# Optimization experiments

Measured on AMD Instinct MI355X. Metric: run time of the kernel, lower is better.

Reference implementation:

```python
import jax, jax.numpy as jnp
import numpy as np

B, C, H, Wd = 4, 64, 64, 64


def setup_inputs() -> dict:
    key = jax.random.key(0)
    k1, k2, k3 = jax.random.split(key, 3)
    x = jax.random.normal(k1, (B, C, H, Wd), dtype=jnp.float32)
    W = jax.random.normal(k2, (C, C), dtype=jnp.float32) * (1.0 / np.sqrt(C))
    b = jax.random.normal(k3, (C,), dtype=jnp.float32) * 0.01
    return {"x": x, "W": W, "b": b}


def reference(x, W, b):
    Bz, Cz, Hz, Wz = x.shape
    N = Hz * Wz
    xf = x.reshape(Bz, Cz, N)                      # values [B,C,N]
    # shared 1x1 conv for queries and keys (same module instance in torch)
    qk = jnp.einsum('oc,bcn->bon', W, xf) + b[None, :, None]  # [B,C,N]
    # scores[b,n,m] = sum_c q[b,c,n] * k[b,c,m], scaled by 1/N
    scores = jnp.einsum('bcn,bcm->bnm', qk, qk) / N           # [B,N,N]
    attn = jax.nn.softmax(scores, axis=-1)                    # softmax over m
    # out[b,c,n] = sum_m values[b,c,m] * attn[b,n,m]
    out = jnp.einsum('bcm,bnm->bcn', xf, attn)
    return out.reshape(Bz, Cz, Hz, Wz)
```

## Files before the change

kernel.cpp:

```cpp
#include <hip/hip_runtime.h>
#include <hip/hip_bf16.h>

#define BATCH 4
#define NSP   4096

typedef __bf16 bf16x8v __attribute__((ext_vector_type(8)));
typedef __bf16 bf16x4v __attribute__((ext_vector_type(4)));
typedef float  floatx4 __attribute__((ext_vector_type(4)));

__global__ __launch_bounds__(256) void qk_kernel(const float* __restrict__ x,
                                                 const float* __restrict__ Wm,
                                                 const float* __restrict__ bias,
                                                 __bf16* __restrict__ qkT) {
    __shared__ __align__(16) __bf16 xT[64 * 72];

    const int t  = threadIdx.x;
    const int b  = blockIdx.x >> 6;
    const int n0 = (blockIdx.x & 63) << 6;

#pragma unroll
    for (int p = 0; p < 4; ++p) {
        const int c  = p * 16 + (t >> 4);
        const int n4 = (t & 15) * 4;
        const float4 v = *(const float4*)(x + (size_t)(b * 64 + c) * 4096 + n0 + n4);
        xT[(n4 + 0) * 72 + c] = (__bf16)(v.x * 0.015625f);
        xT[(n4 + 1) * 72 + c] = (__bf16)(v.y * 0.015625f);
        xT[(n4 + 2) * 72 + c] = (__bf16)(v.z * 0.015625f);
        xT[(n4 + 3) * 72 + c] = (__bf16)(v.w * 0.015625f);
    }
    __syncthreads();

    const int w = t >> 6, lane = t & 63, quad = lane >> 4, l16 = lane & 15;
    const bf16x8v a0 = *(const bf16x8v*)(xT + (w * 16 + l16) * 72 + quad * 8);
    const bf16x8v a1 = *(const bf16x8v*)(xT + (w * 16 + l16) * 72 + 32 + quad * 8);

    floatx4 acc[4];
#pragma unroll
    for (int ot = 0; ot < 4; ++ot) {
        const float* wr = Wm + (ot * 16 + l16) * 64;
        float4 wa = *(const float4*)(wr + quad * 8);
        float4 wb = *(const float4*)(wr + quad * 8 + 4);
        float4 wc = *(const float4*)(wr + 32 + quad * 8);
        float4 wd = *(const float4*)(wr + 32 + quad * 8 + 4);
        bf16x8v b0, b1;
        b0[0]=(__bf16)wa.x; b0[1]=(__bf16)wa.y; b0[2]=(__bf16)wa.z; b0[3]=(__bf16)wa.w;
        b0[4]=(__bf16)wb.x; b0[5]=(__bf16)wb.y; b0[6]=(__bf16)wb.z; b0[7]=(__bf16)wb.w;
        b1[0]=(__bf16)wc.x; b1[1]=(__bf16)wc.y; b1[2]=(__bf16)wc.z; b1[3]=(__bf16)wc.w;
        b1[4]=(__bf16)wd.x; b1[5]=(__bf16)wd.y; b1[6]=(__bf16)wd.z; b1[7]=(__bf16)wd.w;
        acc[ot] = floatx4{0.f, 0.f, 0.f, 0.f};
        acc[ot] = __builtin_amdgcn_mfma_f32_16x16x32_bf16(a0, b0, acc[ot], 0, 0, 0);
        acc[ot] = __builtin_amdgcn_mfma_f32_16x16x32_bf16(a1, b1, acc[ot], 0, 0, 0);
    }
    __syncthreads();

#pragma unroll
    for (int ot = 0; ot < 4; ++ot) {
        const float bo = bias[ot * 16 + l16] * 0.015625f;
#pragma unroll
        for (int r = 0; r < 4; ++r)
            xT[(w * 16 + quad * 4 + r) * 72 + ot * 16 + l16] = (__bf16)(acc[ot][r] + bo);
    }
    __syncthreads();

    const int n = t >> 2, seg = t & 3;
    __bf16* dst = qkT + (size_t)(b * 4096 + n0 + n) * 64 + seg * 16;
    *(bf16x8v*)dst       = *(const bf16x8v*)(xT + n * 72 + seg * 16);
    *(bf16x8v*)(dst + 8) = *(const bf16x8v*)(xT + n * 72 + seg * 16 + 8);
}

template<int SPLIT, int ITERS>
__global__ __launch_bounds__(256, 4) void attn_kernel(const float* __restrict__ x,
                                                      const __bf16* __restrict__ qkT,
                                                      __bf16* __restrict__ Opart,
                                                      float* __restrict__ Lpart) {
    __shared__ __align__(16) char smem[36864];
    __bf16* Klds = (__bf16*)smem;
    __bf16* Vlds = (__bf16*)(smem + 9216);
    __bf16* Plds = (__bf16*)(smem + 18432);
    float*  Olds = (float*)smem;

    const int t   = threadIdx.x;
    const int blk = blockIdx.x;
    const int xcd = blk & 7;
    const int b   = xcd >> 1;
    const int sub = ((blk >> 3) << 1) | (xcd & 1);
    const int qt  = sub / SPLIT;
    const int s   = sub % SPLIT;
    const int n0  = qt << 7;
    const int pblk = (b * 32 + qt) * SPLIT + s;

    const int w = t >> 6, lane = t & 63, quad = lane >> 4, l16 = lane & 15;

    bf16x8v fq[2][2];
#pragma unroll
    for (int qt2 = 0; qt2 < 2; ++qt2) {
        const __bf16* qrow = qkT + (size_t)(b * 4096 + n0 + w * 32 + qt2 * 16 + l16) * 64;
        fq[qt2][0] = *(const bf16x8v*)(qrow + quad * 8);
        fq[qt2][1] = *(const bf16x8v*)(qrow + 32 + quad * 8);
    }

    floatx4 oacc[2][4];
#pragma unroll
    for (int i = 0; i < 2; ++i)
#pragma unroll
        for (int j = 0; j < 4; ++j) oacc[i][j] = floatx4{0.f, 0.f, 0.f, 0.f};
    float rs[2] = {0.f, 0.f};

    for (int it = 0; it < ITERS; ++it) {
        const int m0 = s * (64 * ITERS) + (it << 6);
        __syncthreads();
#pragma unroll
        for (int i = 0; i < 2; ++i) {
            int idx = t + 256 * i;
            int row = idx >> 3, c8 = idx & 7;
            *(uint4*)(Klds + row * 72 + c8 * 8) =
                *(const uint4*)(qkT + (size_t)(b * 4096 + m0 + row) * 64 + c8 * 8);
        }
#pragma unroll
        for (int i = 0; i < 4; ++i) {
            int idx = t + 256 * i;
            int c = idx >> 4, f4 = idx & 15;
            const float4 v = *(const float4*)(x + (size_t)(b * 64 + c) * 4096 + m0 + f4 * 4);
            bf16x4v bv;
            bv[0] = (__bf16)v.x; bv[1] = (__bf16)v.y; bv[2] = (__bf16)v.z; bv[3] = (__bf16)v.w;
            *(bf16x4v*)(Vlds + c * 72 + f4 * 4) = bv;
        }
        __syncthreads();

#pragma unroll
        for (int mt = 0; mt < 4; ++mt) {
            const __bf16* kr = Klds + (mt * 16 + l16) * 72;
            bf16x8v ak0 = *(const bf16x8v*)(kr + quad * 8);
            bf16x8v ak1 = *(const bf16x8v*)(kr + 32 + quad * 8);
#pragma unroll
            for (int qt2 = 0; qt2 < 2; ++qt2) {
                floatx4 sT = {0.f, 0.f, 0.f, 0.f};
                sT = __builtin_amdgcn_mfma_f32_16x16x32_bf16(ak0, fq[qt2][0], sT, 0, 0, 0);
                sT = __builtin_amdgcn_mfma_f32_16x16x32_bf16(ak1, fq[qt2][1], sT, 0, 0, 0);
                float p0 = __expf(sT[0]), p1 = __expf(sT[1]);
                float p2 = __expf(sT[2]), p3 = __expf(sT[3]);
                rs[qt2] += (p0 + p1) + (p2 + p3);
                bf16x4v pv;
                pv[0] = (__bf16)p0; pv[1] = (__bf16)p1; pv[2] = (__bf16)p2; pv[3] = (__bf16)p3;
                *(bf16x4v*)(Plds + (w * 32 + qt2 * 16 + l16) * 72 + mt * 16 + quad * 4) = pv;
            }
        }

        bf16x8v ap[2][2];
#pragma unroll
        for (int qt2 = 0; qt2 < 2; ++qt2) {
            const __bf16* pr = Plds + (w * 32 + qt2 * 16 + l16) * 72;
            ap[qt2][0] = *(const bf16x8v*)(pr + quad * 8);
            ap[qt2][1] = *(const bf16x8v*)(pr + 32 + quad * 8);
        }
#pragma unroll
        for (int ct = 0; ct < 4; ++ct) {
            const __bf16* vr = Vlds + (ct * 16 + l16) * 72;
            bf16x8v bv0 = *(const bf16x8v*)(vr + quad * 8);
            bf16x8v bv1 = *(const bf16x8v*)(vr + 32 + quad * 8);
#pragma unroll
            for (int qt2 = 0; qt2 < 2; ++qt2) {
                oacc[qt2][ct] = __builtin_amdgcn_mfma_f32_16x16x32_bf16(ap[qt2][0], bv0, oacc[qt2][ct], 0, 0, 0);
                oacc[qt2][ct] = __builtin_amdgcn_mfma_f32_16x16x32_bf16(ap[qt2][1], bv1, oacc[qt2][ct], 0, 0, 0);
            }
        }
    }

#pragma unroll
    for (int qt2 = 0; qt2 < 2; ++qt2) {
        float v = rs[qt2];
        v += __shfl_xor(v, 16, 64);
        v += __shfl_xor(v, 32, 64);
        if (quad == 0)
            Lpart[(size_t)pblk * 128 + w * 32 + qt2 * 16 + l16] = v;
    }

    __syncthreads();

#pragma unroll
    for (int qt2 = 0; qt2 < 2; ++qt2)
#pragma unroll
        for (int ct = 0; ct < 4; ++ct)
#pragma unroll
            for (int r = 0; r < 4; ++r)
                Olds[(ct * 16 + l16) * 132 + w * 32 + qt2 * 16 + quad * 4 + r] = oacc[qt2][ct][r];
    __syncthreads();

    const int c = t >> 2, seg = t & 3;
#pragma unroll
    for (int i = 0; i < 4; ++i) {
        floatx4 v0 = *(const floatx4*)(Olds + c * 132 + seg * 32 + i * 8);
        floatx4 v1 = *(const floatx4*)(Olds + c * 132 + seg * 32 + i * 8 + 4);
        bf16x8v pk;
        pk[0]=(__bf16)v0[0]; pk[1]=(__bf16)v0[1]; pk[2]=(__bf16)v0[2]; pk[3]=(__bf16)v0[3];
        pk[4]=(__bf16)v1[0]; pk[5]=(__bf16)v1[1]; pk[6]=(__bf16)v1[2]; pk[7]=(__bf16)v1[3];
        *(bf16x8v*)(Opart + (size_t)pblk * 8192 + c * 128 + seg * 32 + i * 8) = pk;
    }
}

template<int SPLIT>
__global__ __launch_bounds__(256) void reduce_kernel(const __bf16* __restrict__ Opart,
                                                     const float* __restrict__ Lpart,
                                                     float* __restrict__ out) {
    const int blk = blockIdx.x;
    const int bq = blk >> 2, cq = blk & 3;
    const int b = bq >> 5, qt = bq & 31;
    const int t = threadIdx.x;
    const int c  = cq * 16 + (t >> 4);
    const int q8 = (t & 15) * 8;

    float l[8] = {0.f,0.f,0.f,0.f,0.f,0.f,0.f,0.f};
#pragma unroll
    for (int s = 0; s < SPLIT; ++s) {
        const float* lp = Lpart + ((size_t)bq * SPLIT + s) * 128 + q8;
        float4 u = *(const float4*)lp;
        float4 v = *(const float4*)(lp + 4);
        l[0]+=u.x; l[1]+=u.y; l[2]+=u.z; l[3]+=u.w;
        l[4]+=v.x; l[5]+=v.y; l[6]+=v.z; l[7]+=v.w;
    }
    float a[8] = {0.f,0.f,0.f,0.f,0.f,0.f,0.f,0.f};
#pragma unroll
    for (int s = 0; s < SPLIT; ++s) {
        bf16x8v v = *(const bf16x8v*)(Opart + ((size_t)bq * SPLIT + s) * 8192 + c * 128 + q8);
#pragma unroll
        for (int k = 0; k < 8; ++k) a[k] += (float)v[k];
    }
    float* op = out + (size_t)(b * 64 + c) * 4096 + qt * 128 + q8;
    float4 o0, o1;
    o0.x = a[0]/l[0]; o0.y = a[1]/l[1]; o0.z = a[2]/l[2]; o0.w = a[3]/l[3];
    o1.x = a[4]/l[4]; o1.y = a[5]/l[5]; o1.z = a[6]/l[6]; o1.w = a[7]/l[7];
    *(float4*)op       = o0;
    *(float4*)(op + 4) = o1;
}

extern "C" void kernel_launch(void* const* d_in, const int* in_sizes, int n_in,
                              void* d_out, int out_size, void* d_ws, size_t ws_size,
                              hipStream_t stream) {
    const float* x    = (const float*)d_in[0];
    const float* Wm   = (const float*)d_in[1];
    const float* bias = (const float*)d_in[2];
    float* out = (float*)d_out;

    char* ws = (char*)d_ws;
    __bf16* qkT = (__bf16*)ws;

    qk_kernel<<<BATCH * (NSP / 64), 256, 0, stream>>>(x, Wm, bias, qkT);

    const size_t QKT = 2097152;
    const size_t needBig = QKT + (size_t)1024 * 8192 * 2 + (size_t)1024 * 128 * 4;
    if (ws_size >= needBig) {
        __bf16* Opart = (__bf16*)(ws + QKT);
        float*  Lpart = (float*)(ws + QKT + (size_t)1024 * 8192 * 2);
        attn_kernel<8, 8><<<BATCH * 32 * 8, 256, 0, stream>>>(x, qkT, Opart, Lpart);
        reduce_kernel<8><<<512, 256, 0, stream>>>(Opart, Lpart, out);
    } else {
        __bf16* Opart = (__bf16*)(ws + QKT);
        float*  Lpart = (float*)(ws + QKT + (size_t)512 * 8192 * 2);
        attn_kernel<4, 16><<<BATCH * 32 * 4, 256, 0, stream>>>(x, qkT, Opart, Lpart);
        reduce_kernel<4><<<512, 256, 0, stream>>>(Opart, Lpart, out);
    }
}
```

Baseline: 101.4 us.

## Double-buffer K/V tiles, keep P in registers, precompute bf16 values, use exp2

The qk kernel now also writes a bf16 copy of x, so the attention kernel loads V as bf16 directly instead of converting fp32 each tile. K/V staging is double-buffered with register prefetch of the next tile, which removes one barrier per iteration. P no longer goes through LDS: the exp2 results feed the 16x16x16 MFMA directly from registers, and the log2(e) factor is folded into the q/k scale. This costs an extra workspace buffer and a second global write in qk_kernel, and it uses the older 16x16x16 MFMA shape.

```diff
diff --git a/kernel.cpp b/kernel.cpp
--- a/kernel.cpp
+++ b/kernel.cpp
@@ -4,14 +4,40 @@
 #define BATCH 4
 #define NSP   4096
 
+#define QKSCALE 0.0187675376f
+
 typedef __bf16 bf16x8v __attribute__((ext_vector_type(8)));
 typedef __bf16 bf16x4v __attribute__((ext_vector_type(4)));
+typedef short  shortx4 __attribute__((ext_vector_type(4)));
 typedef float  floatx4 __attribute__((ext_vector_type(4)));
+
+static __device__ __forceinline__ shortx4 bf4_bits(bf16x4v v) {
+    union { bf16x4v b; shortx4 s; } u; u.b = v; return u.s;
+}
+
+static __device__ __forceinline__ float fast_exp2(float x) {
+#if __has_builtin(__builtin_amdgcn_exp2f)
+    return __builtin_amdgcn_exp2f(x);
+#else
+    return exp2f(x);
+#endif
+}
+
+static __device__ __forceinline__ floatx4 mfma_pv(shortx4 a, shortx4 b, floatx4 c) {
+#if __has_builtin(__builtin_amdgcn_mfma_f32_16x16x16bf16_1k)
+    return __builtin_amdgcn_mfma_f32_16x16x16bf16_1k(a, b, c, 0, 0, 0);
+#else
+    floatx4 d;
+    asm("v_mfma_f32_16x16x16_bf16 %0, %1, %2, %3" : "=&v"(d) : "v"(a), "v"(b), "v"(c));
+    return d;
+#endif
+}
 
 __global__ __launch_bounds__(256) void qk_kernel(const float* __restrict__ x,
                                                  const float* __restrict__ Wm,
                                                  const float* __restrict__ bias,
-                                                 __bf16* __restrict__ qkT) {
+                                                 __bf16* __restrict__ qkT,
+                                                 __bf16* __restrict__ xbf) {
     __shared__ __align__(16) __bf16 xT[64 * 72];
 
     const int t  = threadIdx.x;
@@ -23,10 +49,13 @@
         const int c  = p * 16 + (t >> 4);
         const int n4 = (t & 15) * 4;
         const float4 v = *(const float4*)(x + (size_t)(b * 64 + c) * 4096 + n0 + n4);
-        xT[(n4 + 0) * 72 + c] = (__bf16)(v.x * 0.015625f);
-        xT[(n4 + 1) * 72 + c] = (__bf16)(v.y * 0.015625f);
-        xT[(n4 + 2) * 72 + c] = (__bf16)(v.z * 0.015625f);
-        xT[(n4 + 3) * 72 + c] = (__bf16)(v.w * 0.015625f);
+        xT[(n4 + 0) * 72 + c] = (__bf16)(v.x * QKSCALE);
+        xT[(n4 + 1) * 72 + c] = (__bf16)(v.y * QKSCALE);
+        xT[(n4 + 2) * 72 + c] = (__bf16)(v.z * QKSCALE);
+        xT[(n4 + 3) * 72 + c] = (__bf16)(v.w * QKSCALE);
+        bf16x4v xv;
+        xv[0] = (__bf16)v.x; xv[1] = (__bf16)v.y; xv[2] = (__bf16)v.z; xv[3] = (__bf16)v.w;
+        *(bf16x4v*)(xbf + (size_t)(b * 64 + c) * 4096 + n0 + n4) = xv;
     }
     __syncthreads();
 
@@ -55,7 +84,7 @@
 
 #pragma unroll
     for (int ot = 0; ot < 4; ++ot) {
-        const float bo = bias[ot * 16 + l16] * 0.015625f;
+        const float bo = bias[ot * 16 + l16] * QKSCALE;
 #pragma unroll
         for (int r = 0; r < 4; ++r)
             xT[(w * 16 + quad * 4 + r) * 72 + ot * 16 + l16] = (__bf16)(acc[ot][r] + bo);
@@ -69,14 +98,13 @@
 }
 
 template<int SPLIT, int ITERS>
-__global__ __launch_bounds__(256, 4) void attn_kernel(const float* __restrict__ x,
+__global__ __launch_bounds__(256, 4) void attn_kernel(const __bf16* __restrict__ xbf,
                                                       const __bf16* __restrict__ qkT,
                                                       __bf16* __restrict__ Opart,
                                                       float* __restrict__ Lpart) {
     __shared__ __align__(16) char smem[36864];
     __bf16* Klds = (__bf16*)smem;
-    __bf16* Vlds = (__bf16*)(smem + 9216);
-    __bf16* Plds = (__bf16*)(smem + 18432);
+    __bf16* Vlds = (__bf16*)(smem + 18432);
     float*  Olds = (float*)smem;
 
     const int t   = threadIdx.x;
@@ -91,10 +119,13 @@
 
     const int w = t >> 6, lane = t & 63, quad = lane >> 4, l16 = lane & 15;
 
+    const __bf16* kgl = qkT + (size_t)b * 4096 * 64;
+    const __bf16* vgl = xbf + (size_t)b * 64 * 4096;
+
     bf16x8v fq[2][2];
 #pragma unroll
     for (int qt2 = 0; qt2 < 2; ++qt2) {
-        const __bf16* qrow = qkT + (size_t)(b * 4096 + n0 + w * 32 + qt2 * 16 + l16) * 64;
+        const __bf16* qrow = kgl + (size_t)(n0 + w * 32 + qt2 * 16 + l16) * 64;
         fq[qt2][0] = *(const bf16x8v*)(qrow + quad * 8);
         fq[qt2][1] = *(const bf16x8v*)(qrow + 32 + quad * 8);
     }
@@ -106,64 +137,64 @@
         for (int j = 0; j < 4; ++j) oacc[i][j] = floatx4{0.f, 0.f, 0.f, 0.f};
     float rs[2] = {0.f, 0.f};
 
+    const int srow = t >> 3;
+    const int sg   = (t & 7) * 8;
+    uint4 kst0, kst1, vst0, vst1;
+    auto stage_load = [&](int m0) {
+        kst0 = *(const uint4*)(kgl + (size_t)(m0 + srow) * 64 + sg);
+        kst1 = *(const uint4*)(kgl + (size_t)(m0 + srow + 32) * 64 + sg);
+        vst0 = *(const uint4*)(vgl + (size_t)srow * 4096 + m0 + sg);
+        vst1 = *(const uint4*)(vgl + (size_t)(srow + 32) * 4096 + m0 + sg);
+    };
+    auto stage_write = [&](int buf) {
+        __bf16* kd = Klds + buf * 4608;
+        __bf16* vd = Vlds + buf * 4608;
+        *(uint4*)(kd + srow * 72 + sg)        = kst0;
+        *(uint4*)(kd + (srow + 32) * 72 + sg) = kst1;
+        *(uint4*)(vd + srow * 72 + sg)        = vst0;
+        *(uint4*)(vd + (srow + 32) * 72 + sg) = vst1;
+    };
+
+    const int mbase = s * (64 * ITERS);
+    stage_load(mbase);
+    stage_write(0);
+    int cur = 0;
+
     for (int it = 0; it < ITERS; ++it) {
-        const int m0 = s * (64 * ITERS) + (it << 6);
+        const int m0 = mbase + (it << 6);
+        if (it + 1 < ITERS) stage_load(m0 + 64);
         __syncthreads();
-#pragma unroll
-        for (int i = 0; i < 2; ++i) {
-            int idx = t + 256 * i;
-            int row = idx >> 3, c8 = idx & 7;
-            *(uint4*)(Klds + row * 72 + c8 * 8) =
-                *(const uint4*)(qkT + (size_t)(b * 4096 + m0 + row) * 64 + c8 * 8);
-        }
-#pragma unroll
-        for (int i = 0; i < 4; ++i) {
-            int idx = t + 256 * i;
-            int c = idx >> 4, f4 = idx & 15;
-            const float4 v = *(const float4*)(x + (size_t)(b * 64 + c) * 4096 + m0 + f4 * 4);
-            bf16x4v bv;
-            bv[0] = (__bf16)v.x; bv[1] = (__bf16)v.y; bv[2] = (__bf16)v.z; bv[3] = (__bf16)v.w;
-            *(bf16x4v*)(Vlds + c * 72 + f4 * 4) = bv;
-        }
-        __syncthreads();
+        const __bf16* Kc = Klds + cur * 4608;
+        const __bf16* Vc = Vlds + cur * 4608;
 
 #pragma unroll
         for (int mt = 0; mt < 4; ++mt) {
-            const __bf16* kr = Klds + (mt * 16 + l16) * 72;
+            const __bf16* kr = Kc + (mt * 16 + l16) * 72;
             bf16x8v ak0 = *(const bf16x8v*)(kr + quad * 8);
             bf16x8v ak1 = *(const bf16x8v*)(kr + 32 + quad * 8);
+            shortx4 pk[2];
 #pragma unroll
             for (int qt2 = 0; qt2 < 2; ++qt2) {
                 floatx4 sT = {0.f, 0.f, 0.f, 0.f};
                 sT = __builtin_amdgcn_mfma_f32_16x16x32_bf16(ak0, fq[qt2][0], sT, 0, 0, 0);
                 sT = __builtin_amdgcn_mfma_f32_16x16x32_bf16(ak1, fq[qt2][1], sT, 0, 0, 0);
-                float p0 = __expf(sT[0]), p1 = __expf(sT[1]);
-                float p2 = __expf(sT[2]), p3 = __expf(sT[3]);
+                float p0 = fast_exp2(sT[0]), p1 = fast_exp2(sT[1]);
+                float p2 = fast_exp2(sT[2]), p3 = fast_exp2(sT[3]);
                 rs[qt2] += (p0 + p1) + (p2 + p3);
                 bf16x4v pv;
                 pv[0] = (__bf16)p0; pv[1] = (__bf16)p1; pv[2] = (__bf16)p2; pv[3] = (__bf16)p3;
-                *(bf16x4v*)(Plds + (w * 32 + qt2 * 16 + l16) * 72 + mt * 16 + quad * 4) = pv;
+                pk[qt2] = bf4_bits(pv);
+            }
+#pragma unroll
+            for (int ct = 0; ct < 4; ++ct) {
+                shortx4 av = *(const shortx4*)(Vc + (ct * 16 + l16) * 72 + mt * 16 + quad * 4);
+                oacc[0][ct] = mfma_pv(av, pk[0], oacc[0][ct]);
+                oacc[1][ct] = mfma_pv(av, pk[1], oacc[1][ct]);
             }
         }
 
-        bf16x8v ap[2][2];
-#pragma unroll
-        for (int qt2 = 0; qt2 < 2; ++qt2) {
-            const __bf16* pr = Plds + (w * 32 + qt2 * 16 + l16) * 72;
-            ap[qt2][0] = *(const bf16x8v*)(pr + quad * 8);
-            ap[qt2][1] = *(const bf16x8v*)(pr + 32 + quad * 8);
-        }
-#pragma unroll
-        for (int ct = 0; ct < 4; ++ct) {
-            const __bf16* vr = Vlds + (ct * 16 + l16) * 72;
-            bf16x8v bv0 = *(const bf16x8v*)(vr + quad * 8);
-            bf16x8v bv1 = *(const bf16x8v*)(vr + 32 + quad * 8);
-#pragma unroll
-            for (int qt2 = 0; qt2 < 2; ++qt2) {
-                oacc[qt2][ct] = __builtin_amdgcn_mfma_f32_16x16x32_bf16(ap[qt2][0], bv0, oacc[qt2][ct], 0, 0, 0);
-                oacc[qt2][ct] = __builtin_amdgcn_mfma_f32_16x16x32_bf16(ap[qt2][1], bv1, oacc[qt2][ct], 0, 0, 0);
-            }
-        }
+        if (it + 1 < ITERS) stage_write(cur ^ 1);
+        cur ^= 1;
     }
 
 #pragma unroll
@@ -183,7 +214,7 @@
         for (int ct = 0; ct < 4; ++ct)
 #pragma unroll
             for (int r = 0; r < 4; ++r)
-                Olds[(ct * 16 + l16) * 132 + w * 32 + qt2 * 16 + quad * 4 + r] = oacc[qt2][ct][r];
+                Olds[(ct * 16 + quad * 4 + r) * 132 + w * 32 + qt2 * 16 + l16] = oacc[qt2][ct][r];
     __syncthreads();
 
     const int c = t >> 2, seg = t & 3;
@@ -243,20 +274,21 @@
 
     char* ws = (char*)d_ws;
     __bf16* qkT = (__bf16*)ws;
-
-    qk_kernel<<<BATCH * (NSP / 64), 256, 0, stream>>>(x, Wm, bias, qkT);
-
-    const size_t QKT = 2097152;
-    const size_t needBig = QKT + (size_t)1024 * 8192 * 2 + (size_t)1024 * 128 * 4;
+    __bf16* xbf = (__bf16*)(ws + 2097152);
+
+    qk_kernel<<<BATCH * (NSP / 64), 256, 0, stream>>>(x, Wm, bias, qkT, xbf);
+
+    const size_t HEAD = 2097152 + 2097152;
+    const size_t needBig = HEAD + (size_t)1024 * 8192 * 2 + (size_t)1024 * 128 * 4;
     if (ws_size >= needBig) {
-        __bf16* Opart = (__bf16*)(ws + QKT);
-        float*  Lpart = (float*)(ws + QKT + (size_t)1024 * 8192 * 2);
-        attn_kernel<8, 8><<<BATCH * 32 * 8, 256, 0, stream>>>(x, qkT, Opart, Lpart);
+        __bf16* Opart = (__bf16*)(ws + HEAD);
+        float*  Lpart = (float*)(ws + HEAD + (size_t)1024 * 8192 * 2);
+        attn_kernel<8, 8><<<BATCH * 32 * 8, 256, 0, stream>>>(xbf, qkT, Opart, Lpart);
         reduce_kernel<8><<<512, 256, 0, stream>>>(Opart, Lpart, out);
     } else {
-        __bf16* Opart = (__bf16*)(ws + QKT);
-        float*  Lpart = (float*)(ws + QKT + (size_t)512 * 8192 * 2);
-        attn_kernel<4, 16><<<BATCH * 32 * 4, 256, 0, stream>>>(x, qkT, Opart, Lpart);
+        __bf16* Opart = (__bf16*)(ws + HEAD);
+        float*  Lpart = (float*)(ws + HEAD + (size_t)512 * 8192 * 2);
+        attn_kernel<4, 16><<<BATCH * 32 * 4, 256, 0, stream>>>(xbf, qkT, Opart, Lpart);
         reduce_kernel<4><<<512, 256, 0, stream>>>(Opart, Lpart, out);
     }
 }
```

Result: faster. 97.27 us (-4.0%).
